# Optimization experiments

Hardware: AMD Instinct MI355X
Metric: run time of the kernel (lower is better)

## Reference

```python
import jax, jax.numpy as jnp
import numpy as np

NUM_HEADS = 8
WINDOW = 8


def _sdpa(q, k, v, scale):
    # q,k,v: (..., heads, S, d)
    scores = jnp.einsum('...sd,...td->...st', q, k) * scale
    p = jax.nn.softmax(scores, axis=-1)
    return jnp.einsum('...st,...td->...sd', p, v)


def setup_inputs() -> dict:
    key = jax.random.key(0)
    k1, k2, k3 = jax.random.split(key, 3)
    B, Himg, Wimg, C = 8, 128, 128, 256
    x = jax.random.normal(k1, (B, Himg * Wimg, C), dtype=jnp.float32)
    W_qkv = jax.random.normal(k2, (C, 3 * C), dtype=jnp.float32) * (C ** -0.5)
    W_proj = jax.random.normal(k3, (C, C), dtype=jnp.float32) * (C ** -0.5)
    b_proj = jnp.zeros((C,), dtype=jnp.float32)
    return {"x": x, "W_qkv": W_qkv, "W_proj": W_proj, "b_proj": b_proj, "H": Himg, "W": Wimg}


def reference(x, W_qkv, W_proj, b_proj, H, W):
    B, N, C = x.shape
    nh, ws = NUM_HEADS, WINDOW
    hd = C // nh
    scale = hd ** -0.5
    split = nh // 2  # local heads = global heads = nh/2

    x4 = x.reshape(B, H, W, C)
    pad_r = (ws - W % ws) % ws
    pad_b = (ws - H % ws) % ws
    if pad_r > 0 or pad_b > 0:
        x4 = jnp.pad(x4, ((0, 0), (0, pad_b), (0, pad_r), (0, 0)))
    Hp, Wp = x4.shape[1], x4.shape[2]

    qkv = (x4 @ W_qkv).reshape(B, Hp, Wp, 3, nh, hd)
    q, k, v = qkv[..., 0, :, :], qkv[..., 1, :, :], qkv[..., 2, :, :]  # (B,Hp,Wp,nh,hd)

    nwh, nww = Hp // ws, Wp // ws

    def win_part(t):
        # (B,Hp,Wp,h,d) -> (B,nwh,nww,h,ws*ws,d)
        h = t.shape[3]
        t = t.reshape(B, nwh, ws, nww, ws, h, hd)
        return t.transpose(0, 1, 3, 5, 2, 4, 6).reshape(B, nwh, nww, h, ws * ws, hd)

    def win_rev(t):
        # (B,nwh,nww,h,ws*ws,d) -> (B,Hp,Wp,h*d)
        h = t.shape[3]
        t = t.reshape(B, nwh, nww, h, ws, ws, hd)
        return t.transpose(0, 1, 4, 2, 5, 3, 6).reshape(B, Hp, Wp, h * hd)

    def grid_part(t):
        # (B,Hp,Wp,h,d) -> (B,ws,ws,h,nwh*nww,d)
        h = t.shape[3]
        t = t.reshape(B, nwh, ws, nww, ws, h, hd)
        return t.transpose(0, 2, 4, 5, 1, 3, 6).reshape(B, ws, ws, h, nwh * nww, hd)

    def grid_rev(t):
        # (B,ws,ws,h,nwh*nww,d) -> (B,Hp,Wp,h*d)
        h = t.shape[3]
        t = t.reshape(B, ws, ws, h, nwh, nww, hd)
        return t.transpose(0, 4, 1, 5, 2, 3, 6).reshape(B, Hp, Wp, h * hd)

    # local branch: first half of heads, window attention
    out_local = win_rev(_sdpa(win_part(q[..., :split, :]),
                              win_part(k[..., :split, :]),
                              win_part(v[..., :split, :]), scale))
    # global branch: second half of heads, grid attention
    out_global = grid_rev(_sdpa(grid_part(q[..., split:, :]),
                                grid_part(k[..., split:, :]),
                                grid_part(v[..., split:, :]), scale))

    out = jnp.concatenate([out_local, out_global], axis=-1)
    if pad_r > 0 or pad_b > 0:
        out = out[:, :H, :W, :]
    out = out.reshape(B, N, C)
    return out @ W_proj + b_proj
```

## Files before the change

kernel.cpp:

```cpp
#include <hip/hip_runtime.h>
#include <hip/hip_bf16.h>

using bf16x8 = __attribute__((ext_vector_type(8))) short;
using f32x4  = __attribute__((ext_vector_type(4))) float;

#define MFMA16(a, b, c) __builtin_amdgcn_mfma_f32_16x16x32_bf16((a), (b), (c), 0, 0, 0)

__device__ __forceinline__ short f2b(float f) {
    unsigned u = __builtin_bit_cast(unsigned, f);
    u = (u + 0x7fffu + ((u >> 16) & 1u)) >> 16;
    return (short)u;
}
__device__ __forceinline__ short pkb(float f) {
    return (short)((__builtin_bit_cast(unsigned, f) + 0x8000u) >> 16);
}
__device__ __forceinline__ unsigned pk2(float lo, float hi) {
    return (unsigned)(unsigned short)pkb(lo) | ((unsigned)(unsigned short)pkb(hi) << 16);
}
__device__ __forceinline__ void gl_lds16(const short* g, short* l) {
    __builtin_amdgcn_global_load_lds(
        (const __attribute__((address_space(1))) unsigned int*)g,
        (__attribute__((address_space(3))) unsigned int*)l, 16, 0, 0);
}

__global__ __launch_bounds__(256)
void cast_x_kernel(const float* __restrict__ x, short* __restrict__ xb) {
    const int i = blockIdx.x * 256 + threadIdx.x;
    const float4 v = ((const float4*)x)[i];
    short4 o;
    o.x = f2b(v.x); o.y = f2b(v.y); o.z = f2b(v.z); o.w = f2b(v.w);
    ((short4*)xb)[i] = o;
}

__global__ __launch_bounds__(256)
void cast_w_kernel(const float* __restrict__ wqkv, const float* __restrict__ wproj,
                   short* __restrict__ wqT, short* __restrict__ wpT) {
    const int t = blockIdx.x * 256 + threadIdx.x;
    if (t < 768 * 256) {
        const int n = t >> 8, k = t & 255;
        float v = wqkv[k * 768 + n];
        if (n < 256) v *= 0.17677669529663687f;
        wqT[t] = f2b(v);
    } else {
        const int u = t - 768 * 256;
        const int n = u >> 8, k = u & 255;
        wpT[u] = f2b(wproj[k * 256 + n]);
    }
}

__global__ __launch_bounds__(256)
void gemm_qkv_kernel(const short* __restrict__ A, const short* __restrict__ Bt,
                     short* __restrict__ qkvL, short* __restrict__ qkvG) {
    __shared__ short As[128 * 32];
    __shared__ short Bs[128 * 32];
    const int tid  = threadIdx.x;
    const int lane = tid & 63, wave = tid >> 6;
    const int wm = wave >> 1, wn = wave & 1;
    const int quad = lane >> 4, l16 = lane & 15;
    const int id = blockIdx.x;
    const int qq = id >> 3, xcd = id & 7;
    const int m0 = (xcd * 128 + qq / 6) * 128;
    const int n0 = (qq % 6) * 128;

    const f32x4 zf = {0.f, 0.f, 0.f, 0.f};
    f32x4 acc[4][4];
#pragma unroll
    for (int i = 0; i < 4; ++i)
#pragma unroll
        for (int j = 0; j < 4; ++j) acc[i][j] = zf;

    const int srow = wave * 16 + (lane >> 2);
    const int scol = (lane & 3) * 8;
    const short* Ap = A  + (long)(m0 + srow) * 256 + scol;
    const short* Bp = Bt + (long)(n0 + srow) * 256 + scol;
    short* lA = &As[wave * 512];
    short* lB = &Bs[wave * 512];

    for (int kt = 0; kt < 8; ++kt) {
        const int off = kt * 32;
        __syncthreads();
        gl_lds16(Ap + off,            lA);
        gl_lds16(Ap + 64 * 256 + off, lA + 2048);
        gl_lds16(Bp + off,            lB);
        gl_lds16(Bp + 64 * 256 + off, lB + 2048);
        __syncthreads();
        bf16x8 af[4], bfr[4];
#pragma unroll
        for (int i = 0; i < 4; ++i)
            af[i] = *(const bf16x8*)&As[(wm * 64 + i * 16 + l16) * 32 + quad * 8];
#pragma unroll
        for (int j = 0; j < 4; ++j)
            bfr[j] = *(const bf16x8*)&Bs[(wn * 64 + j * 16 + l16) * 32 + quad * 8];
#pragma unroll
        for (int i = 0; i < 4; ++i)
#pragma unroll
            for (int j = 0; j < 4; ++j)
                acc[i][j] = MFMA16(af[i], bfr[j], acc[i][j]);
    }

    const int part = n0 >> 8;
    const bool isLocal = ((n0 >> 7) & 1) == 0;
    const bool evenL = (l16 & 1) == 0;
    if (isLocal) {
        short* base = qkvL + part * 2048;
#pragma unroll
        for (int i = 0; i < 4; ++i)
#pragma unroll
            for (int r = 0; r < 4; ++r) {
                const int token = m0 + wm * 64 + i * 16 + quad * 4 + r;
                const int b = token >> 14, hw = token & 16383;
                const int hrow = hw >> 7, wcol = hw & 127;
                const int win = ((hrow >> 3) << 4) + (wcol >> 3);
                const int ti  = ((hrow & 7) << 3) + (wcol & 7);
                const long shb = (long)((b << 8) + win) << 2;
#pragma unroll
                for (int j = 0; j < 4; ++j) {
                    const float v = acc[i][j][r];
                    const float w = __shfl_xor(v, 1);
                    if (evenL) {
                        const int c128 = wn * 64 + j * 16 + l16;
                        const int head = c128 >> 5, ch = c128 & 31;
                        *(unsigned*)&base[(shb + head) * 6144 + ti * 32 + ch] = pk2(v, w);
                    }
                }
            }
    } else {
        short* base = qkvG + part * 8192;
#pragma unroll
        for (int i = 0; i < 4; ++i)
#pragma unroll
            for (int r = 0; r < 4; ++r) {
                const int token = m0 + wm * 64 + i * 16 + quad * 4 + r;
                const int b = token >> 14, hw = token & 16383;
                const int hrow = hw >> 7, wcol = hw & 127;
                const int pos = ((hrow & 7) << 3) + (wcol & 7);
                const int ti  = ((hrow >> 3) << 4) + (wcol >> 3);
                const long shb = (long)((b << 6) + pos) << 2;
#pragma unroll
                for (int j = 0; j < 4; ++j) {
                    const float v = acc[i][j][r];
                    const float w = __shfl_xor(v, 1);
                    if (evenL) {
                        const int c128 = wn * 64 + j * 16 + l16;
                        const int head = c128 >> 5, ch = c128 & 31;
                        *(unsigned*)&base[(shb + head) * 24576 + ti * 32 + ch] = pk2(v, w);
                    }
                }
            }
    }
}

__global__ __launch_bounds__(256)
void gemm_proj_kernel(const short* __restrict__ A, const short* __restrict__ Bt,
                      float* __restrict__ C, const float* __restrict__ bias) {
    __shared__ short As[128 * 32];
    __shared__ short Bs[128 * 32];
    const int tid  = threadIdx.x;
    const int lane = tid & 63, wave = tid >> 6;
    const int wm = wave >> 1, wn = wave & 1;
    const int quad = lane >> 4, l16 = lane & 15;
    const int id = blockIdx.x;
    const int qq = id >> 3, xcd = id & 7;
    const int m0 = (xcd * 128 + (qq >> 1)) * 128;
    const int n0 = (qq & 1) * 128;

    const f32x4 zf = {0.f, 0.f, 0.f, 0.f};
    f32x4 acc[4][4];
#pragma unroll
    for (int i = 0; i < 4; ++i)
#pragma unroll
        for (int j = 0; j < 4; ++j) acc[i][j] = zf;

    const int srow = wave * 16 + (lane >> 2);
    const int scol = (lane & 3) * 8;
    const short* Ap = A  + (long)(m0 + srow) * 256 + scol;
    const short* Bp = Bt + (long)(n0 + srow) * 256 + scol;
    short* lA = &As[wave * 512];
    short* lB = &Bs[wave * 512];

    for (int kt = 0; kt < 8; ++kt) {
        const int off = kt * 32;
        __syncthreads();
        gl_lds16(Ap + off,            lA);
        gl_lds16(Ap + 64 * 256 + off, lA + 2048);
        gl_lds16(Bp + off,            lB);
        gl_lds16(Bp + 64 * 256 + off, lB + 2048);
        __syncthreads();
        bf16x8 af[4], bfr[4];
#pragma unroll
        for (int i = 0; i < 4; ++i)
            af[i] = *(const bf16x8*)&As[(wm * 64 + i * 16 + l16) * 32 + quad * 8];
#pragma unroll
        for (int j = 0; j < 4; ++j)
            bfr[j] = *(const bf16x8*)&Bs[(wn * 64 + j * 16 + l16) * 32 + quad * 8];
#pragma unroll
        for (int i = 0; i < 4; ++i)
#pragma unroll
            for (int j = 0; j < 4; ++j)
                acc[i][j] = MFMA16(af[i], bfr[j], acc[i][j]);
    }

#pragma unroll
    for (int i = 0; i < 4; ++i)
#pragma unroll
        for (int r = 0; r < 4; ++r) {
            const long row = m0 + wm * 64 + i * 16 + quad * 4 + r;
#pragma unroll
            for (int j = 0; j < 4; ++j) {
                const int col = n0 + wn * 64 + j * 16 + l16;
                C[row * 256 + col] = acc[i][j][r] + bias[col];
            }
        }
}

__global__ __launch_bounds__(256)
void local_attn_kernel(const short* __restrict__ qkvL, short* __restrict__ attn) {
    __shared__ short sVT[4][32 * 72];
    __shared__ short sP[4][16 * 72];
    const int tid  = threadIdx.x;
    const int lane = tid & 63, wave = tid >> 6;
    const int quad = lane >> 4, l16 = lane & 15;
    const int sh   = blockIdx.x * 4 + wave;
    const int head = sh & 3;
    const int win  = (sh >> 2) & 255;
    const int b    = sh >> 10;
    const int base_tok = b * 16384 + (win >> 4) * 1024 + (win & 15) * 8;
    const int ch = head * 32;
    const short* qb = qkvL + (long)sh * 6144;
    const short* kb = qb + 2048;
    const short* vp = qb + 4096;

    {
        bf16x8 v0 = *(const bf16x8*)(vp + lane * 32);
        bf16x8 v1 = *(const bf16x8*)(vp + lane * 32 + 8);
        bf16x8 v2 = *(const bf16x8*)(vp + lane * 32 + 16);
        bf16x8 v3 = *(const bf16x8*)(vp + lane * 32 + 24);
#pragma unroll
        for (int d = 0; d < 8; ++d) {
            sVT[wave][(d     ) * 72 + lane] = v0[d];
            sVT[wave][(d +  8) * 72 + lane] = v1[d];
            sVT[wave][(d + 16) * 72 + lane] = v2[d];
            sVT[wave][(d + 24) * 72 + lane] = v3[d];
        }
    }
    __syncthreads();

    bf16x8 aq[4], bk[4];
#pragma unroll
    for (int i = 0; i < 4; ++i)
        aq[i] = *(const bf16x8*)(qb + (i * 16 + l16) * 32 + quad * 8);
#pragma unroll
    for (int j = 0; j < 4; ++j)
        bk[j] = *(const bf16x8*)(kb + (j * 16 + l16) * 32 + quad * 8);

    bf16x8 vbf[2][2];
#pragma unroll
    for (int kk = 0; kk < 2; ++kk)
#pragma unroll
        for (int j2 = 0; j2 < 2; ++j2)
            vbf[kk][j2] = *(const bf16x8*)&sVT[wave][(j2 * 16 + l16) * 72 + kk * 32 + quad * 8];

    const bf16x8 vone = {0x3F80, 0x3F80, 0x3F80, 0x3F80, 0x3F80, 0x3F80, 0x3F80, 0x3F80};
    const f32x4 zf = {0.f, 0.f, 0.f, 0.f};
    const bool evenL = (l16 & 1) == 0;

#pragma unroll
    for (int i = 0; i < 4; ++i) {
        f32x4 sa[4] = {zf, zf, zf, zf};
#pragma unroll
        for (int j = 0; j < 4; ++j)
            sa[j] = MFMA16(aq[i], bk[j], sa[j]);
#pragma unroll
        for (int j = 0; j < 4; ++j)
#pragma unroll
            for (int r = 0; r < 4; ++r)
                sP[wave][(quad * 4 + r) * 72 + j * 16 + l16] = pkb(__expf(sa[j][r]));
        __syncthreads();

        f32x4 o0 = zf, o1 = zf, os = zf;
#pragma unroll
        for (int kk = 0; kk < 2; ++kk) {
            const bf16x8 pa = *(const bf16x8*)&sP[wave][l16 * 72 + kk * 32 + quad * 8];
            o0 = MFMA16(pa, vbf[kk][0], o0);
            o1 = MFMA16(pa, vbf[kk][1], o1);
            os = MFMA16(pa, vone, os);
        }
        __syncthreads();

#pragma unroll
        for (int r = 0; r < 4; ++r) {
            const int s = i * 16 + quad * 4 + r;
            const int tok = base_tok + (s >> 3) * 128 + (s & 7);
            const float inv = 1.f / os[r];
            const float a0 = o0[r] * inv, a1 = o1[r] * inv;
            const float b0 = __shfl_xor(a0, 1), b1 = __shfl_xor(a1, 1);
            if (evenL) {
                *(unsigned*)&attn[(long)tok * 256 + ch + l16]      = pk2(a0, b0);
                *(unsigned*)&attn[(long)tok * 256 + ch + 16 + l16] = pk2(a1, b1);
            }
        }
    }
}

__global__ __launch_bounds__(256)
void global_attn_kernel(const short* __restrict__ qkvG, short* __restrict__ attn) {
    __shared__ short sVT[32 * 264];
    __shared__ short sP[4][16 * 72];
    const int tid  = threadIdx.x;
    const int lane = tid & 63, wave = tid >> 6;
    const int quad = lane >> 4, l16 = lane & 15;
    const int sh   = blockIdx.x;
    const int head = sh & 3;
    const int pos  = (sh >> 2) & 63;
    const int b    = sh >> 8;
    const int base_tok = b * 16384 + (pos >> 3) * 128 + (pos & 7);
    const int ch = (4 + head) * 32;
    const short* qb = qkvG + (long)sh * 24576;
    const short* kb = qb + 8192;
    const short* vp = qb + 16384;

    {
        bf16x8 v0 = *(const bf16x8*)(vp + tid * 32);
        bf16x8 v1 = *(const bf16x8*)(vp + tid * 32 + 8);
        bf16x8 v2 = *(const bf16x8*)(vp + tid * 32 + 16);
        bf16x8 v3 = *(const bf16x8*)(vp + tid * 32 + 24);
#pragma unroll
        for (int d = 0; d < 8; ++d) {
            sVT[(d     ) * 264 + tid] = v0[d];
            sVT[(d +  8) * 264 + tid] = v1[d];
            sVT[(d + 16) * 264 + tid] = v2[d];
            sVT[(d + 24) * 264 + tid] = v3[d];
        }
    }
    __syncthreads();

    bf16x8 aq[4];
#pragma unroll
    for (int i = 0; i < 4; ++i)
        aq[i] = *(const bf16x8*)(qb + (wave * 64 + i * 16 + l16) * 32 + quad * 8);

    const bf16x8 vone = {0x3F80, 0x3F80, 0x3F80, 0x3F80, 0x3F80, 0x3F80, 0x3F80, 0x3F80};
    const f32x4 zf = {0.f, 0.f, 0.f, 0.f};
    f32x4 o0[4], o1[4], os[4];
#pragma unroll
    for (int i = 0; i < 4; ++i) { o0[i] = zf; o1[i] = zf; os[i] = zf; }

    for (int nc = 0; nc < 4; ++nc) {
        bf16x8 bk[4];
#pragma unroll
        for (int j = 0; j < 4; ++j)
            bk[j] = *(const bf16x8*)(kb + (nc * 64 + j * 16 + l16) * 32 + quad * 8);
        bf16x8 vbf[2][2];
#pragma unroll
        for (int kk = 0; kk < 2; ++kk)
#pragma unroll
            for (int j2 = 0; j2 < 2; ++j2)
                vbf[kk][j2] = *(const bf16x8*)&sVT[(j2 * 16 + l16) * 264 + nc * 64 + kk * 32 + quad * 8];

#pragma unroll
        for (int i = 0; i < 4; ++i) {
            f32x4 sa[4] = {zf, zf, zf, zf};
#pragma unroll
            for (int j = 0; j < 4; ++j)
                sa[j] = MFMA16(aq[i], bk[j], sa[j]);
#pragma unroll
            for (int j = 0; j < 4; ++j)
#pragma unroll
                for (int r = 0; r < 4; ++r)
                    sP[wave][(quad * 4 + r) * 72 + j * 16 + l16] = pkb(__expf(sa[j][r]));
            __syncthreads();
#pragma unroll
            for (int kk = 0; kk < 2; ++kk) {
                const bf16x8 pa = *(const bf16x8*)&sP[wave][l16 * 72 + kk * 32 + quad * 8];
                o0[i] = MFMA16(pa, vbf[kk][0], o0[i]);
                o1[i] = MFMA16(pa, vbf[kk][1], o1[i]);
                os[i] = MFMA16(pa, vone, os[i]);
            }
            __syncthreads();
        }
    }

    const bool evenL = (l16 & 1) == 0;
#pragma unroll
    for (int i = 0; i < 4; ++i)
#pragma unroll
        for (int r = 0; r < 4; ++r) {
            const int s = wave * 64 + i * 16 + quad * 4 + r;
            const int tok = base_tok + (s >> 4) * 1024 + (s & 15) * 8;
            const float inv = 1.f / os[i][r];
            const float a0 = o0[i][r] * inv, a1 = o1[i][r] * inv;
            const float b0 = __shfl_xor(a0, 1), b1 = __shfl_xor(a1, 1);
            if (evenL) {
                *(unsigned*)&attn[(long)tok * 256 + ch + l16]      = pk2(a0, b0);
                *(unsigned*)&attn[(long)tok * 256 + ch + 16 + l16] = pk2(a1, b1);
            }
        }
}

extern "C" void kernel_launch(void* const* d_in, const int* in_sizes, int n_in,
                              void* d_out, int out_size, void* d_ws, size_t ws_size,
                              hipStream_t stream) {
    const float* x     = (const float*)d_in[0];
    const float* wqkv  = (const float*)d_in[1];
    const float* wproj = (const float*)d_in[2];
    const float* bproj = (const float*)d_in[3];

    char* ws = (char*)d_ws;
    short* xb   = (short*)(ws);
    short* wqT  = (short*)(ws +  67108864);
    short* wpT  = (short*)(ws +  67502080);
    short* qkvL = (short*)(ws +  67633152);
    short* qkvG = (short*)(ws + 168296448);
    short* attn = (short*)(ws + 268959744);
    float* out  = (float*)d_out;

    cast_x_kernel<<<dim3(32768), dim3(256), 0, stream>>>(x, xb);
    cast_w_kernel<<<dim3(1024), dim3(256), 0, stream>>>(wqkv, wproj, wqT, wpT);
    gemm_qkv_kernel<<<dim3(6144), dim3(256), 0, stream>>>(xb, wqT, qkvL, qkvG);
    local_attn_kernel<<<dim3(2048), dim3(256), 0, stream>>>(qkvL, attn);
    global_attn_kernel<<<dim3(2048), dim3(256), 0, stream>>>(qkvG, attn);
    gemm_proj_kernel<<<dim3(2048), dim3(256), 0, stream>>>(attn, wpT, out, bproj);
}
```

Baseline: 483.5 us.

## Stage QKV GEMM output through LDS for coalesced scatter; drop per-wave barriers

The QKV GEMM epilogue now writes the bf16 accumulator tile into a padded shared-memory buffer and then copies it to the window- and grid-partitioned layouts with wide 8- or 16-byte contiguous stores, replacing scattered 4-byte stores that needed a shuffle. The attention kernels also drop the block-wide __syncthreads around the per-wave sP scratch buffer, since each wave only touches its own slice. This trades a larger LDS footprint in the GEMM, which can lower occupancy, for better store coalescing and fewer barriers. Removing the barriers depends on wave-level ordering of LDS accesses, which is not guaranteed without at least a wave barrier or a memory fence.

```diff
diff --git a/kernel.cpp b/kernel.cpp
--- a/kernel.cpp
+++ b/kernel.cpp
@@ -51,8 +51,9 @@
 __global__ __launch_bounds__(256)
 void gemm_qkv_kernel(const short* __restrict__ A, const short* __restrict__ Bt,
                      short* __restrict__ qkvL, short* __restrict__ qkvG) {
-    __shared__ short As[128 * 32];
-    __shared__ short Bs[128 * 32];
+    __shared__ __align__(16) short smem[128 * 136];
+    short* As = smem;
+    short* Bs = smem + 4096;
     const int tid  = threadIdx.x;
     const int lane = tid & 63, wave = tid >> 6;
     const int wm = wave >> 1, wn = wave & 1;
@@ -98,55 +99,53 @@
                 acc[i][j] = MFMA16(af[i], bfr[j], acc[i][j]);
     }
 
+    __syncthreads();
+    short* Cs = smem;
+    {
+        const int crow = wm * 64 + quad * 4;
+        const int ccol = wn * 64 + l16;
+#pragma unroll
+        for (int i = 0; i < 4; ++i)
+#pragma unroll
+            for (int j = 0; j < 4; ++j)
+#pragma unroll
+                for (int r = 0; r < 4; ++r)
+                    Cs[(crow + i * 16 + r) * 136 + ccol + j * 16] = pkb(acc[i][j][r]);
+    }
+    __syncthreads();
+
     const int part = n0 >> 8;
     const bool isLocal = ((n0 >> 7) & 1) == 0;
-    const bool evenL = (l16 & 1) == 0;
+    const int b    = m0 >> 14;
+    const int hrow = (m0 >> 7) & 127;
     if (isLocal) {
-        short* base = qkvL + part * 2048;
-#pragma unroll
-        for (int i = 0; i < 4; ++i)
-#pragma unroll
-            for (int r = 0; r < 4; ++r) {
-                const int token = m0 + wm * 64 + i * 16 + quad * 4 + r;
-                const int b = token >> 14, hw = token & 16383;
-                const int hrow = hw >> 7, wcol = hw & 127;
-                const int win = ((hrow >> 3) << 4) + (wcol >> 3);
-                const int ti  = ((hrow & 7) << 3) + (wcol & 7);
-                const long shb = (long)((b << 8) + win) << 2;
-#pragma unroll
-                for (int j = 0; j < 4; ++j) {
-                    const float v = acc[i][j][r];
-                    const float w = __shfl_xor(v, 1);
-                    if (evenL) {
-                        const int c128 = wn * 64 + j * 16 + l16;
-                        const int head = c128 >> 5, ch = c128 & 31;
-                        *(unsigned*)&base[(shb + head) * 6144 + ti * 32 + ch] = pk2(v, w);
-                    }
-                }
-            }
+        short* dst0 = qkvL + part * 2048;
+        const int win_hi = (hrow >> 3) << 4;
+        const int ti0    = (hrow & 7) * 8;
+        const int t  = lane >> 3;
+        const int s4 = (lane & 7) * 4;
+#pragma unroll
+        for (int c = 0; c < 16; ++c) {
+            const int idx = wave * 16 + c;
+            const int wi = idx >> 2, h = idx & 3;
+            const ushort4 v = *(const ushort4*)&Cs[(wi * 8 + t) * 136 + h * 32 + s4];
+            short* dp = dst0 + (long)(((b << 8) | (win_hi | wi)) * 4 + h) * 6144 + ti0 * 32;
+            *(ushort4*)&dp[lane * 4] = v;
+        }
     } else {
-        short* base = qkvG + part * 8192;
-#pragma unroll
-        for (int i = 0; i < 4; ++i)
-#pragma unroll
-            for (int r = 0; r < 4; ++r) {
-                const int token = m0 + wm * 64 + i * 16 + quad * 4 + r;
-                const int b = token >> 14, hw = token & 16383;
-                const int hrow = hw >> 7, wcol = hw & 127;
-                const int pos = ((hrow & 7) << 3) + (wcol & 7);
-                const int ti  = ((hrow >> 3) << 4) + (wcol >> 3);
-                const long shb = (long)((b << 6) + pos) << 2;
-#pragma unroll
-                for (int j = 0; j < 4; ++j) {
-                    const float v = acc[i][j][r];
-                    const float w = __shfl_xor(v, 1);
-                    if (evenL) {
-                        const int c128 = wn * 64 + j * 16 + l16;
-                        const int head = c128 >> 5, ch = c128 & 31;
-                        *(unsigned*)&base[(shb + head) * 24576 + ti * 32 + ch] = pk2(v, w);
-                    }
-                }
-            }
+        short* dst0 = qkvG + part * 8192;
+        const int pos0 = (hrow & 7) * 8;
+        const int tib  = (hrow >> 3) * 16;
+        const int tt = lane >> 2;
+        const int s8 = (lane & 3) * 8;
+#pragma unroll
+        for (int c = 0; c < 8; ++c) {
+            const int idx = wave * 8 + c;
+            const int p = idx >> 2, h = idx & 3;
+            const bf16x8 v = *(const bf16x8*)&Cs[(p + tt * 8) * 136 + h * 32 + s8];
+            short* dp = dst0 + (long)(((b << 6) | (pos0 + p)) * 4 + h) * 24576 + tib * 32;
+            *(bf16x8*)&dp[lane * 8] = v;
+        }
     }
 }
 
@@ -275,7 +274,6 @@
 #pragma unroll
             for (int r = 0; r < 4; ++r)
                 sP[wave][(quad * 4 + r) * 72 + j * 16 + l16] = pkb(__expf(sa[j][r]));
-        __syncthreads();
 
         f32x4 o0 = zf, o1 = zf, os = zf;
 #pragma unroll
@@ -285,7 +283,6 @@
             o1 = MFMA16(pa, vbf[kk][1], o1);
             os = MFMA16(pa, vone, os);
         }
-        __syncthreads();
 
 #pragma unroll
         for (int r = 0; r < 4; ++r) {
@@ -368,7 +365,6 @@
 #pragma unroll
                 for (int r = 0; r < 4; ++r)
                     sP[wave][(quad * 4 + r) * 72 + j * 16 + l16] = pkb(__expf(sa[j][r]));
-            __syncthreads();
 #pragma unroll
             for (int kk = 0; kk < 2; ++kk) {
                 const bf16x8 pa = *(const bf16x8*)&sP[wave][l16 * 72 + kk * 32 + quad * 8];
@@ -376,7 +372,6 @@
                 o1[i] = MFMA16(pa, vbf[kk][1], o1[i]);
                 os[i] = MFMA16(pa, vone, os[i]);
             }
-            __syncthreads();
         }
     }
 
```

New measurement: 449.2 us. -7.1%, faster.
